# Optimization experiments

Measured on AMD Instinct MI355X. Metric: run time of the kernel, lower is better.

## Reference

```python
import jax, jax.numpy as jnp
import numpy as np

N, D_IN, UNITS = 8192, 2048, 2048


def setup_inputs() -> dict:
    key = jax.random.key(0)
    ks = jax.random.split(key, 14)
    s_in = 1.0 / np.sqrt(D_IN)
    s_u = 1.0 / np.sqrt(UNITS)
    return {
        "x": jax.random.normal(ks[0], (N, UNITS), jnp.float32),
        "y": jax.random.normal(ks[1], (N, D_IN), jnp.float32),
        # W* act on y (D_IN -> UNITS), U* act on x (UNITS -> UNITS)
        "Wz": jax.random.normal(ks[2], (D_IN, UNITS), jnp.float32) * s_in,
        "bz": jnp.zeros((UNITS,), jnp.float32),
        "Uz": jax.random.normal(ks[3], (UNITS, UNITS), jnp.float32) * s_u,
        "buz": jax.random.normal(ks[4], (UNITS,), jnp.float32) * 0.05,  # glorot-init bias
        "Wr": jax.random.normal(ks[5], (D_IN, UNITS), jnp.float32) * s_in,
        "br": jnp.zeros((UNITS,), jnp.float32),
        "Ur": jax.random.normal(ks[6], (UNITS, UNITS), jnp.float32) * s_u,
        "bur": jnp.zeros((UNITS,), jnp.float32),
        "Wg": jax.random.normal(ks[7], (D_IN, UNITS), jnp.float32) * s_in,
        "bg": jax.random.normal(ks[8], (UNITS,), jnp.float32) * 0.05,  # glorot-init bias
        "Ug": jax.random.normal(ks[9], (UNITS, UNITS), jnp.float32) * s_u,
        "bug": jnp.zeros((UNITS,), jnp.float32),
    }


def reference(x, y, Wz, bz, Uz, buz, Wr, br, Ur, bur, Wg, bg, Ug, bug):
    # Batch the three y-projections and the two x-projections into single GEMMs.
    Wy = y @ jnp.concatenate([Wz, Wr, Wg], axis=1)          # [N, 3*UNITS]
    Ux = x @ jnp.concatenate([Uz, Ur], axis=1)               # [N, 2*UNITS]
    u = Wz.shape[1]
    z = Wy[:, :u] + bz + Ux[:, :u] + buz                     # NOTE: no sigmoid (faithful to source)
    r = Wy[:, u:2 * u] + br + Ux[:, u:] + bur                # NOTE: no sigmoid (faithful to source)
    h = jnp.tanh(Wy[:, 2 * u:] + bg + (r * x) @ Ug + bug)
    return (1.0 - z) * x + z * h
```

## Files before the change

### kernel.cpp

```cpp
#include <hip/hip_runtime.h>
#include <hip/hip_bf16.h>
#include <cstdint>
#include <cmath>

typedef __bf16 bf16;
typedef __bf16 bf16x8 __attribute__((ext_vector_type(8)));
typedef __bf16 bf16x4 __attribute__((ext_vector_type(4)));
typedef __bf16 bf16x2 __attribute__((ext_vector_type(2)));
typedef float f32x4 __attribute__((ext_vector_type(4)));

#define NROWS 8192
#define UNITS 2048
#define NT 64
#define NSPLIT 32

__device__ __forceinline__ void gload_lds16(const bf16* g, const bf16* lds) {
  __builtin_amdgcn_global_load_lds(
      (const __attribute__((address_space(1))) uint32_t*)(uintptr_t)g,
      (__attribute__((address_space(3))) uint32_t*)(uint32_t)(uintptr_t)lds,
      16, 0, 0);
}

#define BARR do { asm volatile("" ::: "memory"); __builtin_amdgcn_s_barrier(); \
                  asm volatile("" ::: "memory"); } while (0)
#define SCHEDB do { asm volatile("" ::: "memory"); __builtin_amdgcn_sched_barrier(0); \
                    asm volatile("" ::: "memory"); } while (0)
#define WAITV(N) asm volatile("s_waitcnt vmcnt(" #N ")" ::: "memory")

__device__ __forceinline__ float fast_tanh(float v) {
  float e = __expf(2.f * v);
  return 1.f - 2.f / (e + 1.f);
}

__global__ void pack_xy_kernel(const float* __restrict__ x, const float* __restrict__ y,
                               bf16* __restrict__ xb, bf16* __restrict__ yb) {
  size_t n4 = (size_t)NROWS * UNITS / 4;
  size_t stride = (size_t)gridDim.x * blockDim.x;
  for (size_t i = (size_t)blockIdx.x * blockDim.x + threadIdx.x; i < n4; i += stride) {
    float4 vx = ((const float4*)x)[i];
    float4 vy = ((const float4*)y)[i];
    bf16x4 ox = {(bf16)vx.x, (bf16)vx.y, (bf16)vx.z, (bf16)vx.w};
    bf16x4 oy = {(bf16)vy.x, (bf16)vy.y, (bf16)vy.z, (bf16)vy.w};
    ((bf16x4*)xb)[i] = ox;
    ((bf16x4*)yb)[i] = oy;
  }
}

__global__ void transpose_cvt6_kernel(const float* __restrict__ Wz, const float* __restrict__ Uz,
                                      const float* __restrict__ Wr, const float* __restrict__ Ur,
                                      const float* __restrict__ Wg, const float* __restrict__ Ug,
                                      bf16* __restrict__ Bzr, bf16* __restrict__ Bgt) {
  __shared__ float t[64][33];
  const float* src;
  bf16* dst;
  int koff;
  switch (blockIdx.z) {
    case 0: src = Wz; dst = Bzr;                         koff = 0;    break;
    case 1: src = Uz; dst = Bzr;                         koff = 2048; break;
    case 2: src = Wr; dst = Bzr + (size_t)2048 * 4096;   koff = 0;    break;
    case 3: src = Ur; dst = Bzr + (size_t)2048 * 4096;   koff = 2048; break;
    case 4: src = Wg; dst = Bgt;                         koff = 0;    break;
    default: src = Ug; dst = Bgt;                        koff = 2048; break;
  }
  int j0 = blockIdx.x * 32, k0 = blockIdx.y * 64;
  int tx = threadIdx.x & 31, ty = threadIdx.x >> 5;
#pragma unroll
  for (int i = 0; i < 64; i += 8)
    t[ty + i][tx] = src[(size_t)(k0 + ty + i) * UNITS + j0 + tx];
  __syncthreads();
#pragma unroll
  for (int i = 0; i < 32; i += 8) {
    int j = j0 + ty + i;
    bf16x2 v = {(bf16)t[2 * tx][ty + i], (bf16)t[2 * tx + 1][ty + i]};
    *(bf16x2*)&dst[(size_t)j * 4096 + koff + k0 + 2 * tx] = v;
  }
}

template <int EPI>
__global__ __launch_bounds__(512, 2)
void gemm256(const bf16* __restrict__ A0, const bf16* __restrict__ A1,
             const bf16* __restrict__ Bt,
             const float* __restrict__ bias_a, const float* __restrict__ bias_b,
             const float* __restrict__ bias_c, const float* __restrict__ bias_d,
             const bf16* __restrict__ xin, bf16* __restrict__ zbuf,
             bf16* __restrict__ rxbuf, float* __restrict__ outbuf) {
  __shared__ bf16 LDS[2][32768];
  const int tid = threadIdx.x;
  const int wv = tid >> 6, lane = tid & 63;
  const int wr = wv >> 2, wc = wv & 3;

  const int nl = (int)gridDim.x >> 3;
  const int xc = (int)blockIdx.x & 7;
  const int l = (int)blockIdx.x >> 3;
  const int bxq = nl >> 4;
  const int by = (xc & 1) * 16 + (l & 15);
  const int bx = (xc >> 1) * bxq + (l >> 4);
  const int brow = by * 256;
  const int bcol = bx * 256;

  const int rr = lane >> 2;
  const int kk_st = ((lane & 3) * 8) ^ ((rr & 6) << 2);
  int offA[2][2], offB[2][2], dstA[2][2], dstB[2][2];
#pragma unroll
  for (int H = 0; H < 2; ++H)
#pragma unroll
    for (int c = 0; c < 2; ++c) {
      int ssA = H * 8 + wv;
      offA[H][c] = (brow + c * 128 + (ssA >> 1) * 16 + rr) * 2048 + (ssA & 1) * 32 + kk_st;
      dstA[H][c] = c * 8192 + ssA * 512;
      int ssB = (wv >> 2) * 8 + H * 4 + (wv & 3);
      offB[H][c] = (bcol + c * 128 + (ssB >> 1) * 16 + rr) * 4096 + (ssB & 1) * 32 + kk_st;
      dstB[H][c] = 16384 + c * 8192 + ssB * 512;
    }

  const int lr = lane & 15;
  const int kread = ((lane >> 4) * 8) ^ ((lr & 6) << 2);
  const int abase = wr * 8192 + lr * 32 + kread;
  const int bbase = 16384 + (wc >> 1) * 8192 + (wc & 1) * 4096 + lr * 32 + kread;

#define ST_A(TI, H, BUF)                                                      \
  if ((TI) < NT) {                                                            \
    const bf16* _s = ((TI) < NSPLIT) ? A0 + (size_t)(TI)*64                   \
                                     : A1 + (size_t)((TI)-NSPLIT) * 64;       \
    gload_lds16(_s + offA[H][0], (BUF) + dstA[H][0]);                         \
    gload_lds16(_s + offA[H][1], (BUF) + dstA[H][1]);                         \
  }
#define ST_B(TI, H, BUF)                                                      \
  if ((TI) < NT) {                                                            \
    const bf16* _s = Bt + (size_t)(TI)*64;                                    \
    gload_lds16(_s + offB[H][0], (BUF) + dstB[H][0]);                         \
    gload_lds16(_s + offB[H][1], (BUF) + dstB[H][1]);                         \
  }
#define RD_B(DST, LP, NB)                                                     \
  _Pragma("unroll") for (int kh = 0; kh < 2; ++kh)                            \
  _Pragma("unroll") for (int n = 0; n < 2; ++n)                               \
      DST[n][kh] = *(const bf16x8*)((LP) + bbase + ((n + 2 * (NB)) * 2 + kh) * 512);
#define RD_A(DST, LP, MB)                                                     \
  _Pragma("unroll") for (int kh = 0; kh < 2; ++kh)                            \
  _Pragma("unroll") for (int m = 0; m < 4; ++m)                               \
      DST[m][kh] = *(const bf16x8*)((LP) + abase + ((m + 4 * (MB)) * 2 + kh) * 512);
#define MFMA_Q(AARR, BARR_, MOFF, NOFF)                                       \
  __builtin_amdgcn_s_setprio(1);                                              \
  _Pragma("unroll") for (int kh = 0; kh < 2; ++kh)                            \
  _Pragma("unroll") for (int m = 0; m < 4; ++m)                               \
  _Pragma("unroll") for (int n = 0; n < 2; ++n)                               \
      acc[m + MOFF][n + NOFF] = __builtin_amdgcn_mfma_f32_16x16x32_bf16(      \
          AARR[m][kh], BARR_[n][kh], acc[m + MOFF][n + NOFF], 0, 0, 0);       \
  __builtin_amdgcn_s_setprio(0);

  f32x4 acc[8][4];
#pragma unroll
  for (int m = 0; m < 8; ++m)
#pragma unroll
    for (int n = 0; n < 4; ++n) {
      f32x4 zz = {0.f, 0.f, 0.f, 0.f};
      acc[m][n] = zz;
    }

  bf16x8 a0[4][2], a1[4][2], b0[2][2], b1[2][2];

  {
    bf16* L0 = &LDS[0][0];
    bf16* L1 = &LDS[1][0];
    ST_A(0, 0, L0); ST_B(0, 0, L0); ST_A(0, 1, L0); ST_B(0, 1, L0);
    ST_B(1, 0, L1); ST_A(1, 0, L1);
    WAITV(4);
    BARR;
  }

#define TILE(T, CUR, NXT, WB)                                                 \
  {                                                                           \
    const bf16* Lc = &LDS[CUR][0];                                            \
    bf16* Lcw = &LDS[CUR][0];                                                 \
    bf16* Lnw = &LDS[NXT][0];                                                 \
                                                                     \
    ST_A((T) + 1, 1, Lnw);                                                    \
    ST_B((T) + 1, 1, Lnw);                                                    \
    RD_A(a0, Lc, 0);                                                          \
    RD_B(b0, Lc, 0);                                                          \
    RD_B(b1, Lc, 1);                                                          \
    SCHEDB;                                                                   \
    MFMA_Q(a0, b0, 0, 0);                                                     \
    MFMA_Q(a0, b1, 0, 2);                                                     \
    BARR;                                                                     \
                                                                     \
    ST_B((T) + 2, 0, Lcw);                                                    \
    ST_A((T) + 2, 0, Lcw);                                                    \
    RD_A(a1, Lc, 1);                                                          \
    SCHEDB;                                                                   \
    MFMA_Q(a1, b0, 4, 0);                                                     \
    MFMA_Q(a1, b1, 4, 2);                                                     \
    WAITV(WB); BARR;                                                          \
  }

#pragma unroll 1
  for (int t = 0; t < NT - 2; t += 2) {
    TILE(t, 0, 1, 4);
    TILE(t + 1, 1, 0, 4);
  }
  TILE(NT - 2, 0, 1, 0);
  TILE(NT - 1, 1, 0, 0);

  const int lq = (lane >> 4) << 2;
  const int lc = lane & 15;
  const int rowb = brow + wr * 128;
  const int colb = bcol + wc * 64;
  if constexpr (EPI == 0) {
    if (bcol < UNITS) {
#pragma unroll
      for (int m = 0; m < 8; ++m)
#pragma unroll
        for (int n = 0; n < 4; ++n) {
          int col = colb + n * 16 + lc;
          float ba = bias_a[col] + bias_b[col];
#pragma unroll
          for (int q = 0; q < 4; ++q) {
            int row = rowb + m * 16 + lq + q;
            zbuf[(size_t)row * UNITS + col] = (bf16)(acc[m][n][q] + ba);
          }
        }
    } else {
#pragma unroll
      for (int m = 0; m < 8; ++m)
#pragma unroll
        for (int n = 0; n < 4; ++n) {
          int col = colb - UNITS + n * 16 + lc;
          float bc = bias_c[col] + bias_d[col];
#pragma unroll
          for (int q = 0; q < 4; ++q) {
            int row = rowb + m * 16 + lq + q;
            size_t idx = (size_t)row * UNITS + col;
            float r = acc[m][n][q] + bc;
            rxbuf[idx] = (bf16)(r * (float)xin[idx]);
          }
        }
    }
  } else {
#pragma unroll
    for (int m = 0; m < 8; ++m)
#pragma unroll
      for (int n = 0; n < 4; ++n) {
        int col = colb + n * 16 + lc;
        float bg_ = bias_a[col] + bias_b[col];
#pragma unroll
        for (int q = 0; q < 4; ++q) {
          int row = rowb + m * 16 + lq + q;
          size_t idx = (size_t)row * UNITS + col;
          float h = fast_tanh(acc[m][n][q] + bg_);
          float zv = (float)zbuf[idx];
          float xv = (float)xin[idx];
          outbuf[idx] = (1.f - zv) * xv + zv * h;
        }
      }
  }
#undef ST_A
#undef ST_B
#undef RD_A
#undef RD_B
#undef MFMA_Q
#undef TILE
}

extern "C" void kernel_launch(void* const* d_in, const int* in_sizes, int n_in,
                              void* d_out, int out_size, void* d_ws, size_t ws_size,
                              hipStream_t stream) {
  const float* x   = (const float*)d_in[0];
  const float* y   = (const float*)d_in[1];
  const float* Wz  = (const float*)d_in[2];
  const float* bz  = (const float*)d_in[3];
  const float* Uz  = (const float*)d_in[4];
  const float* buz = (const float*)d_in[5];
  const float* Wr  = (const float*)d_in[6];
  const float* br  = (const float*)d_in[7];
  const float* Ur  = (const float*)d_in[8];
  const float* bur = (const float*)d_in[9];
  const float* Wg  = (const float*)d_in[10];
  const float* bg  = (const float*)d_in[11];
  const float* Ug  = (const float*)d_in[12];
  const float* bug = (const float*)d_in[13];
  float* out = (float*)d_out;

  char* w = (char*)d_ws;
  bf16* Ybf = (bf16*)w;  w += (size_t)NROWS * UNITS * 2;
  bf16* Xbf = (bf16*)w;  w += (size_t)NROWS * UNITS * 2;
  bf16* RX  = (bf16*)w;  w += (size_t)NROWS * UNITS * 2;
  bf16* Bzr = (bf16*)w;  w += (size_t)4096 * 4096 * 2;
  bf16* Bgt = (bf16*)w;  w += (size_t)2048 * 4096 * 2;
  bf16* Zb  = (bf16*)w;  w += (size_t)NROWS * UNITS * 2;

  pack_xy_kernel<<<2048, 256, 0, stream>>>(x, y, Xbf, Ybf);
  dim3 tg(64, 32, 6);
  transpose_cvt6_kernel<<<tg, 256, 0, stream>>>(Wz, Uz, Wr, Ur, Wg, Ug, Bzr, Bgt);

  gemm256<0><<<512, 512, 0, stream>>>(Ybf, Xbf, Bzr, bz, buz, br, bur, Xbf, Zb, RX, nullptr);
  gemm256<1><<<256, 512, 0, stream>>>(Ybf, RX, Bgt, bg, bug, nullptr, nullptr, Xbf, Zb, nullptr, out);
}
```

Baseline: 421.5 us.

## Use 16 waves per 256x256 GEMM tile, halving per-wave work

Doubles the workgroup to 1024 threads (16 waves in a 4x4 arrangement), so each wave owns a 64x64 sub-tile instead of 128x64. The global-to-LDS staging is reassigned so each wave issues one 16-byte load per half instead of two, and the wait counts are adjusted to match. The aim is more latency hiding per CU and lower accumulator register pressure. In exchange the LDS reuse ratio per wave drops, there are more barrier participants, and occupancy drops to one block per CU at 128KB LDS.

```diff
diff --git a/kernel.cpp b/kernel.cpp
--- a/kernel.cpp
+++ b/kernel.cpp
@@ -77,7 +77,7 @@
 }
 
 template <int EPI>
-__global__ __launch_bounds__(512, 2)
+__global__ __launch_bounds__(1024)
 void gemm256(const bf16* __restrict__ A0, const bf16* __restrict__ A1,
              const bf16* __restrict__ Bt,
              const float* __restrict__ bias_a, const float* __restrict__ bias_b,
@@ -86,8 +86,9 @@
              bf16* __restrict__ rxbuf, float* __restrict__ outbuf) {
   __shared__ bf16 LDS[2][32768];
   const int tid = threadIdx.x;
-  const int wv = tid >> 6, lane = tid & 63;
-  const int wr = wv >> 2, wc = wv & 3;
+  const int lane = tid & 63;
+  const int wvu = __builtin_amdgcn_readfirstlane(tid >> 6);
+  const int wr = wvu >> 2, wc = wvu & 3;
 
   const int nl = (int)gridDim.x >> 3;
   const int xc = (int)blockIdx.x & 7;
@@ -100,36 +101,33 @@
 
   const int rr = lane >> 2;
   const int kk_st = ((lane & 3) * 8) ^ ((rr & 6) << 2);
-  int offA[2][2], offB[2][2], dstA[2][2], dstB[2][2];
-#pragma unroll
-  for (int H = 0; H < 2; ++H)
-#pragma unroll
-    for (int c = 0; c < 2; ++c) {
-      int ssA = H * 8 + wv;
-      offA[H][c] = (brow + c * 128 + (ssA >> 1) * 16 + rr) * 2048 + (ssA & 1) * 32 + kk_st;
-      dstA[H][c] = c * 8192 + ssA * 512;
-      int ssB = (wv >> 2) * 8 + H * 4 + (wv & 3);
-      offB[H][c] = (bcol + c * 128 + (ssB >> 1) * 16 + rr) * 4096 + (ssB & 1) * 32 + kk_st;
-      dstB[H][c] = 16384 + c * 8192 + ssB * 512;
-    }
+  const int laneA = rr * 2048 + kk_st;
+  const int laneB = rr * 4096 + kk_st;
+  int uniA[2], uniB[2], dstA[2], dstB[2];
+#pragma unroll
+  for (int H = 0; H < 2; ++H) {
+    int ss = (wvu >> 2) * 8 + H * 4 + (wvu & 3);
+    uniA[H] = (brow + (ss >> 1) * 16) * 2048 + (ss & 1) * 32;
+    dstA[H] = ss * 512;
+    uniB[H] = (bcol + (ss >> 1) * 16) * 4096 + (ss & 1) * 32;
+    dstB[H] = 16384 + ss * 512;
+  }
 
   const int lr = lane & 15;
   const int kread = ((lane >> 4) * 8) ^ ((lr & 6) << 2);
-  const int abase = wr * 8192 + lr * 32 + kread;
-  const int bbase = 16384 + (wc >> 1) * 8192 + (wc & 1) * 4096 + lr * 32 + kread;
+  const int abase = wr * 4096 + lr * 32 + kread;
+  const int bbase = 16384 + wc * 4096 + lr * 32 + kread;
 
 #define ST_A(TI, H, BUF)                                                      \
   if ((TI) < NT) {                                                            \
     const bf16* _s = ((TI) < NSPLIT) ? A0 + (size_t)(TI)*64                   \
                                      : A1 + (size_t)((TI)-NSPLIT) * 64;       \
-    gload_lds16(_s + offA[H][0], (BUF) + dstA[H][0]);                         \
-    gload_lds16(_s + offA[H][1], (BUF) + dstA[H][1]);                         \
+    gload_lds16(_s + uniA[H] + laneA, (BUF) + dstA[H]);                       \
   }
 #define ST_B(TI, H, BUF)                                                      \
   if ((TI) < NT) {                                                            \
     const bf16* _s = Bt + (size_t)(TI)*64;                                    \
-    gload_lds16(_s + offB[H][0], (BUF) + dstB[H][0]);                         \
-    gload_lds16(_s + offB[H][1], (BUF) + dstB[H][1]);                         \
+    gload_lds16(_s + uniB[H] + laneB, (BUF) + dstB[H]);                       \
   }
 #define RD_B(DST, LP, NB)                                                     \
   _Pragma("unroll") for (int kh = 0; kh < 2; ++kh)                            \
@@ -137,34 +135,34 @@
       DST[n][kh] = *(const bf16x8*)((LP) + bbase + ((n + 2 * (NB)) * 2 + kh) * 512);
 #define RD_A(DST, LP, MB)                                                     \
   _Pragma("unroll") for (int kh = 0; kh < 2; ++kh)                            \
-  _Pragma("unroll") for (int m = 0; m < 4; ++m)                               \
-      DST[m][kh] = *(const bf16x8*)((LP) + abase + ((m + 4 * (MB)) * 2 + kh) * 512);
+  _Pragma("unroll") for (int m = 0; m < 2; ++m)                               \
+      DST[m][kh] = *(const bf16x8*)((LP) + abase + ((m + 2 * (MB)) * 2 + kh) * 512);
 #define MFMA_Q(AARR, BARR_, MOFF, NOFF)                                       \
   __builtin_amdgcn_s_setprio(1);                                              \
   _Pragma("unroll") for (int kh = 0; kh < 2; ++kh)                            \
-  _Pragma("unroll") for (int m = 0; m < 4; ++m)                               \
+  _Pragma("unroll") for (int m = 0; m < 2; ++m)                               \
   _Pragma("unroll") for (int n = 0; n < 2; ++n)                               \
       acc[m + MOFF][n + NOFF] = __builtin_amdgcn_mfma_f32_16x16x32_bf16(      \
           AARR[m][kh], BARR_[n][kh], acc[m + MOFF][n + NOFF], 0, 0, 0);       \
   __builtin_amdgcn_s_setprio(0);
 
-  f32x4 acc[8][4];
-#pragma unroll
-  for (int m = 0; m < 8; ++m)
+  f32x4 acc[4][4];
+#pragma unroll
+  for (int m = 0; m < 4; ++m)
 #pragma unroll
     for (int n = 0; n < 4; ++n) {
       f32x4 zz = {0.f, 0.f, 0.f, 0.f};
       acc[m][n] = zz;
     }
 
-  bf16x8 a0[4][2], a1[4][2], b0[2][2], b1[2][2];
+  bf16x8 a0[2][2], a1[2][2], b0[2][2], b1[2][2];
 
   {
     bf16* L0 = &LDS[0][0];
     bf16* L1 = &LDS[1][0];
     ST_A(0, 0, L0); ST_B(0, 0, L0); ST_A(0, 1, L0); ST_B(0, 1, L0);
     ST_B(1, 0, L1); ST_A(1, 0, L1);
-    WAITV(4);
+    WAITV(2);
     BARR;
   }
 
@@ -188,27 +186,27 @@
     ST_A((T) + 2, 0, Lcw);                                                    \
     RD_A(a1, Lc, 1);                                                          \
     SCHEDB;                                                                   \
-    MFMA_Q(a1, b0, 4, 0);                                                     \
-    MFMA_Q(a1, b1, 4, 2);                                                     \
+    MFMA_Q(a1, b0, 2, 0);                                                     \
+    MFMA_Q(a1, b1, 2, 2);                                                     \
     WAITV(WB); BARR;                                                          \
   }
 
 #pragma unroll 1
   for (int t = 0; t < NT - 2; t += 2) {
-    TILE(t, 0, 1, 4);
-    TILE(t + 1, 1, 0, 4);
+    TILE(t, 0, 1, 2);
+    TILE(t + 1, 1, 0, 2);
   }
   TILE(NT - 2, 0, 1, 0);
   TILE(NT - 1, 1, 0, 0);
 
   const int lq = (lane >> 4) << 2;
   const int lc = lane & 15;
-  const int rowb = brow + wr * 128;
+  const int rowb = brow + wr * 64;
   const int colb = bcol + wc * 64;
   if constexpr (EPI == 0) {
     if (bcol < UNITS) {
 #pragma unroll
-      for (int m = 0; m < 8; ++m)
+      for (int m = 0; m < 4; ++m)
 #pragma unroll
         for (int n = 0; n < 4; ++n) {
           int col = colb + n * 16 + lc;
@@ -221,7 +219,7 @@
         }
     } else {
 #pragma unroll
-      for (int m = 0; m < 8; ++m)
+      for (int m = 0; m < 4; ++m)
 #pragma unroll
         for (int n = 0; n < 4; ++n) {
           int col = colb - UNITS + n * 16 + lc;
@@ -237,7 +235,7 @@
     }
   } else {
 #pragma unroll
-    for (int m = 0; m < 8; ++m)
+    for (int m = 0; m < 4; ++m)
 #pragma unroll
       for (int n = 0; n < 4; ++n) {
         int col = colb + n * 16 + lc;
@@ -292,6 +290,6 @@
   dim3 tg(64, 32, 6);
   transpose_cvt6_kernel<<<tg, 256, 0, stream>>>(Wz, Uz, Wr, Ur, Wg, Ug, Bzr, Bgt);
 
-  gemm256<0><<<512, 512, 0, stream>>>(Ybf, Xbf, Bzr, bz, buz, br, bur, Xbf, Zb, RX, nullptr);
-  gemm256<1><<<256, 512, 0, stream>>>(Ybf, RX, Bgt, bg, bug, nullptr, nullptr, Xbf, Zb, nullptr, out);
-}
+  gemm256<0><<<512, 1024, 0, stream>>>(Ybf, Xbf, Bzr, bz, buz, br, bur, Xbf, Zb, RX, nullptr);
+  gemm256<1><<<256, 1024, 0, stream>>>(Ybf, RX, Bgt, bg, bug, nullptr, nullptr, Xbf, Zb, nullptr, out);
+}
```

Result: no change. 425.9 us (+1.0%).

## Use 16-wave 1024-thread blocks for the first fused GEMM

Applied to the files above, without the earlier changes.

Adds a gemm16w variant that computes each 256x256 tile with 16 waves of 64x64 instead of 8 waves of 128x64. Each wave now issues one global->LDS load per half-stage instead of two, and holds half the accumulator and A-fragment registers. The first GEMM launches with 1024 threads per block while the second keeps the original 8-wave kernel. This cuts per-wave register pressure and adds more waves to hide latency, at the cost of more LDS B-fragment reads per MFMA and only one block per CU given the 128KB LDS footprint.

```diff
diff --git a/kernel.cpp b/kernel.cpp
--- a/kernel.cpp
+++ b/kernel.cpp
@@ -77,8 +77,8 @@
 }
 
 template <int EPI>
-__global__ __launch_bounds__(512, 2)
-void gemm256(const bf16* __restrict__ A0, const bf16* __restrict__ A1,
+__global__ __launch_bounds__(1024)
+void gemm16w(const bf16* __restrict__ A0, const bf16* __restrict__ A1,
              const bf16* __restrict__ Bt,
              const float* __restrict__ bias_a, const float* __restrict__ bias_b,
              const float* __restrict__ bias_c, const float* __restrict__ bias_d,
@@ -86,8 +86,9 @@
              bf16* __restrict__ rxbuf, float* __restrict__ outbuf) {
   __shared__ bf16 LDS[2][32768];
   const int tid = threadIdx.x;
-  const int wv = tid >> 6, lane = tid & 63;
-  const int wr = wv >> 2, wc = wv & 3;
+  const int lane = tid & 63;
+  const int wvu = __builtin_amdgcn_readfirstlane(tid >> 6);
+  const int wr = wvu >> 2, wc = wvu & 3;
 
   const int nl = (int)gridDim.x >> 3;
   const int xc = (int)blockIdx.x & 7;
@@ -100,36 +101,33 @@
 
   const int rr = lane >> 2;
   const int kk_st = ((lane & 3) * 8) ^ ((rr & 6) << 2);
-  int offA[2][2], offB[2][2], dstA[2][2], dstB[2][2];
-#pragma unroll
-  for (int H = 0; H < 2; ++H)
-#pragma unroll
-    for (int c = 0; c < 2; ++c) {
-      int ssA = H * 8 + wv;
-      offA[H][c] = (brow + c * 128 + (ssA >> 1) * 16 + rr) * 2048 + (ssA & 1) * 32 + kk_st;
-      dstA[H][c] = c * 8192 + ssA * 512;
-      int ssB = (wv >> 2) * 8 + H * 4 + (wv & 3);
-      offB[H][c] = (bcol + c * 128 + (ssB >> 1) * 16 + rr) * 4096 + (ssB & 1) * 32 + kk_st;
-      dstB[H][c] = 16384 + c * 8192 + ssB * 512;
-    }
+  const int laneA = rr * 2048 + kk_st;
+  const int laneB = rr * 4096 + kk_st;
+  int uniA[2], uniB[2], dstA[2], dstB[2];
+#pragma unroll
+  for (int H = 0; H < 2; ++H) {
+    int ss = (wvu >> 2) * 8 + H * 4 + (wvu & 3);
+    uniA[H] = (brow + (ss >> 1) * 16) * 2048 + (ss & 1) * 32;
+    dstA[H] = ss * 512;
+    uniB[H] = (bcol + (ss >> 1) * 16) * 4096 + (ss & 1) * 32;
+    dstB[H] = 16384 + ss * 512;
+  }
 
   const int lr = lane & 15;
   const int kread = ((lane >> 4) * 8) ^ ((lr & 6) << 2);
-  const int abase = wr * 8192 + lr * 32 + kread;
-  const int bbase = 16384 + (wc >> 1) * 8192 + (wc & 1) * 4096 + lr * 32 + kread;
+  const int abase = wr * 4096 + lr * 32 + kread;
+  const int bbase = 16384 + wc * 4096 + lr * 32 + kread;
 
 #define ST_A(TI, H, BUF)                                                      \
   if ((TI) < NT) {                                                            \
     const bf16* _s = ((TI) < NSPLIT) ? A0 + (size_t)(TI)*64                   \
                                      : A1 + (size_t)((TI)-NSPLIT) * 64;       \
-    gload_lds16(_s + offA[H][0], (BUF) + dstA[H][0]);                         \
-    gload_lds16(_s + offA[H][1], (BUF) + dstA[H][1]);                         \
+    gload_lds16(_s + uniA[H] + laneA, (BUF) + dstA[H]);                       \
   }
 #define ST_B(TI, H, BUF)                                                      \
   if ((TI) < NT) {                                                            \
     const bf16* _s = Bt + (size_t)(TI)*64;                                    \
-    gload_lds16(_s + offB[H][0], (BUF) + dstB[H][0]);                         \
-    gload_lds16(_s + offB[H][1], (BUF) + dstB[H][1]);                         \
+    gload_lds16(_s + uniB[H] + laneB, (BUF) + dstB[H]);                       \
   }
 #define RD_B(DST, LP, NB)                                                     \
   _Pragma("unroll") for (int kh = 0; kh < 2; ++kh)                            \
@@ -137,34 +135,34 @@
       DST[n][kh] = *(const bf16x8*)((LP) + bbase + ((n + 2 * (NB)) * 2 + kh) * 512);
 #define RD_A(DST, LP, MB)                                                     \
   _Pragma("unroll") for (int kh = 0; kh < 2; ++kh)                            \
-  _Pragma("unroll") for (int m = 0; m < 4; ++m)                               \
-      DST[m][kh] = *(const bf16x8*)((LP) + abase + ((m + 4 * (MB)) * 2 + kh) * 512);
+  _Pragma("unroll") for (int m = 0; m < 2; ++m)                               \
+      DST[m][kh] = *(const bf16x8*)((LP) + abase + ((m + 2 * (MB)) * 2 + kh) * 512);
 #define MFMA_Q(AARR, BARR_, MOFF, NOFF)                                       \
   __builtin_amdgcn_s_setprio(1);                                              \
   _Pragma("unroll") for (int kh = 0; kh < 2; ++kh)                            \
-  _Pragma("unroll") for (int m = 0; m < 4; ++m)                               \
+  _Pragma("unroll") for (int m = 0; m < 2; ++m)                               \
   _Pragma("unroll") for (int n = 0; n < 2; ++n)                               \
       acc[m + MOFF][n + NOFF] = __builtin_amdgcn_mfma_f32_16x16x32_bf16(      \
           AARR[m][kh], BARR_[n][kh], acc[m + MOFF][n + NOFF], 0, 0, 0);       \
   __builtin_amdgcn_s_setprio(0);
 
-  f32x4 acc[8][4];
-#pragma unroll
-  for (int m = 0; m < 8; ++m)
+  f32x4 acc[4][4];
+#pragma unroll
+  for (int m = 0; m < 4; ++m)
 #pragma unroll
     for (int n = 0; n < 4; ++n) {
       f32x4 zz = {0.f, 0.f, 0.f, 0.f};
       acc[m][n] = zz;
     }
 
-  bf16x8 a0[4][2], a1[4][2], b0[2][2], b1[2][2];
+  bf16x8 a0[2][2], a1[2][2], b0[2][2], b1[2][2];
 
   {
     bf16* L0 = &LDS[0][0];
     bf16* L1 = &LDS[1][0];
     ST_A(0, 0, L0); ST_B(0, 0, L0); ST_A(0, 1, L0); ST_B(0, 1, L0);
     ST_B(1, 0, L1); ST_A(1, 0, L1);
-    WAITV(4);
+    WAITV(2);
     BARR;
   }
 
@@ -173,7 +171,6 @@
     const bf16* Lc = &LDS[CUR][0];                                            \
     bf16* Lcw = &LDS[CUR][0];                                                 \
     bf16* Lnw = &LDS[NXT][0];                                                 \
-                                                                     \
     ST_A((T) + 1, 1, Lnw);                                                    \
     ST_B((T) + 1, 1, Lnw);                                                    \
     RD_A(a0, Lc, 0);                                                          \
@@ -183,7 +180,189 @@
     MFMA_Q(a0, b0, 0, 0);                                                     \
     MFMA_Q(a0, b1, 0, 2);                                                     \
     BARR;                                                                     \
-                                                                     \
+    ST_B((T) + 2, 0, Lcw);                                                    \
+    ST_A((T) + 2, 0, Lcw);                                                    \
+    RD_A(a1, Lc, 1);                                                          \
+    SCHEDB;                                                                   \
+    MFMA_Q(a1, b0, 2, 0);                                                     \
+    MFMA_Q(a1, b1, 2, 2);                                                     \
+    WAITV(WB); BARR;                                                          \
+  }
+
+#pragma unroll 1
+  for (int t = 0; t < NT - 2; t += 2) {
+    TILE(t, 0, 1, 2);
+    TILE(t + 1, 1, 0, 2);
+  }
+  TILE(NT - 2, 0, 1, 0);
+  TILE(NT - 1, 1, 0, 0);
+
+  const int lq = (lane >> 4) << 2;
+  const int lc = lane & 15;
+  const int rowb = brow + wr * 64;
+  const int colb = bcol + wc * 64;
+  if constexpr (EPI == 0) {
+    if (bcol < UNITS) {
+#pragma unroll
+      for (int m = 0; m < 4; ++m)
+#pragma unroll
+        for (int n = 0; n < 4; ++n) {
+          int col = colb + n * 16 + lc;
+          float ba = bias_a[col] + bias_b[col];
+#pragma unroll
+          for (int q = 0; q < 4; ++q) {
+            int row = rowb + m * 16 + lq + q;
+            zbuf[(size_t)row * UNITS + col] = (bf16)(acc[m][n][q] + ba);
+          }
+        }
+    } else {
+#pragma unroll
+      for (int m = 0; m < 4; ++m)
+#pragma unroll
+        for (int n = 0; n < 4; ++n) {
+          int col = colb - UNITS + n * 16 + lc;
+          float bc = bias_c[col] + bias_d[col];
+#pragma unroll
+          for (int q = 0; q < 4; ++q) {
+            int row = rowb + m * 16 + lq + q;
+            size_t idx = (size_t)row * UNITS + col;
+            float r = acc[m][n][q] + bc;
+            rxbuf[idx] = (bf16)(r * (float)xin[idx]);
+          }
+        }
+    }
+  } else {
+#pragma unroll
+    for (int m = 0; m < 4; ++m)
+#pragma unroll
+      for (int n = 0; n < 4; ++n) {
+        int col = colb + n * 16 + lc;
+        float bg_ = bias_a[col] + bias_b[col];
+#pragma unroll
+        for (int q = 0; q < 4; ++q) {
+          int row = rowb + m * 16 + lq + q;
+          size_t idx = (size_t)row * UNITS + col;
+          float h = fast_tanh(acc[m][n][q] + bg_);
+          float zv = (float)zbuf[idx];
+          float xv = (float)xin[idx];
+          outbuf[idx] = (1.f - zv) * xv + zv * h;
+        }
+      }
+  }
+#undef ST_A
+#undef ST_B
+#undef RD_A
+#undef RD_B
+#undef MFMA_Q
+#undef TILE
+}
+
+template <int EPI>
+__global__ __launch_bounds__(512, 2)
+void gemm8w(const bf16* __restrict__ A0, const bf16* __restrict__ A1,
+            const bf16* __restrict__ Bt,
+            const float* __restrict__ bias_a, const float* __restrict__ bias_b,
+            const float* __restrict__ bias_c, const float* __restrict__ bias_d,
+            const bf16* __restrict__ xin, bf16* __restrict__ zbuf,
+            bf16* __restrict__ rxbuf, float* __restrict__ outbuf) {
+  __shared__ bf16 LDS[2][32768];
+  const int tid = threadIdx.x;
+  const int wv = tid >> 6, lane = tid & 63;
+  const int wr = wv >> 2, wc = wv & 3;
+
+  const int nl = (int)gridDim.x >> 3;
+  const int xc = (int)blockIdx.x & 7;
+  const int l = (int)blockIdx.x >> 3;
+  const int bxq = nl >> 4;
+  const int by = (xc & 1) * 16 + (l & 15);
+  const int bx = (xc >> 1) * bxq + (l >> 4);
+  const int brow = by * 256;
+  const int bcol = bx * 256;
+
+  const int rr = lane >> 2;
+  const int kk_st = ((lane & 3) * 8) ^ ((rr & 6) << 2);
+  int offA[2][2], offB[2][2], dstA[2][2], dstB[2][2];
+#pragma unroll
+  for (int H = 0; H < 2; ++H)
+#pragma unroll
+    for (int c = 0; c < 2; ++c) {
+      int ssA = H * 8 + wv;
+      offA[H][c] = (brow + c * 128 + (ssA >> 1) * 16 + rr) * 2048 + (ssA & 1) * 32 + kk_st;
+      dstA[H][c] = c * 8192 + ssA * 512;
+      int ssB = (wv >> 2) * 8 + H * 4 + (wv & 3);
+      offB[H][c] = (bcol + c * 128 + (ssB >> 1) * 16 + rr) * 4096 + (ssB & 1) * 32 + kk_st;
+      dstB[H][c] = 16384 + c * 8192 + ssB * 512;
+    }
+
+  const int lr = lane & 15;
+  const int kread = ((lane >> 4) * 8) ^ ((lr & 6) << 2);
+  const int abase = wr * 8192 + lr * 32 + kread;
+  const int bbase = 16384 + (wc >> 1) * 8192 + (wc & 1) * 4096 + lr * 32 + kread;
+
+#define ST_A(TI, H, BUF)                                                      \
+  if ((TI) < NT) {                                                            \
+    const bf16* _s = ((TI) < NSPLIT) ? A0 + (size_t)(TI)*64                   \
+                                     : A1 + (size_t)((TI)-NSPLIT) * 64;       \
+    gload_lds16(_s + offA[H][0], (BUF) + dstA[H][0]);                         \
+    gload_lds16(_s + offA[H][1], (BUF) + dstA[H][1]);                         \
+  }
+#define ST_B(TI, H, BUF)                                                      \
+  if ((TI) < NT) {                                                            \
+    const bf16* _s = Bt + (size_t)(TI)*64;                                    \
+    gload_lds16(_s + offB[H][0], (BUF) + dstB[H][0]);                         \
+    gload_lds16(_s + offB[H][1], (BUF) + dstB[H][1]);                         \
+  }
+#define RD_B(DST, LP, NB)                                                     \
+  _Pragma("unroll") for (int kh = 0; kh < 2; ++kh)                            \
+  _Pragma("unroll") for (int n = 0; n < 2; ++n)                               \
+      DST[n][kh] = *(const bf16x8*)((LP) + bbase + ((n + 2 * (NB)) * 2 + kh) * 512);
+#define RD_A(DST, LP, MB)                                                     \
+  _Pragma("unroll") for (int kh = 0; kh < 2; ++kh)                            \
+  _Pragma("unroll") for (int m = 0; m < 4; ++m)                               \
+      DST[m][kh] = *(const bf16x8*)((LP) + abase + ((m + 4 * (MB)) * 2 + kh) * 512);
+#define MFMA_Q(AARR, BARR_, MOFF, NOFF)                                       \
+  __builtin_amdgcn_s_setprio(1);                                              \
+  _Pragma("unroll") for (int kh = 0; kh < 2; ++kh)                            \
+  _Pragma("unroll") for (int m = 0; m < 4; ++m)                               \
+  _Pragma("unroll") for (int n = 0; n < 2; ++n)                               \
+      acc[m + MOFF][n + NOFF] = __builtin_amdgcn_mfma_f32_16x16x32_bf16(      \
+          AARR[m][kh], BARR_[n][kh], acc[m + MOFF][n + NOFF], 0, 0, 0);       \
+  __builtin_amdgcn_s_setprio(0);
+
+  f32x4 acc[8][4];
+#pragma unroll
+  for (int m = 0; m < 8; ++m)
+#pragma unroll
+    for (int n = 0; n < 4; ++n) {
+      f32x4 zz = {0.f, 0.f, 0.f, 0.f};
+      acc[m][n] = zz;
+    }
+
+  bf16x8 a0[4][2], a1[4][2], b0[2][2], b1[2][2];
+
+  {
+    bf16* L0 = &LDS[0][0];
+    bf16* L1 = &LDS[1][0];
+    ST_A(0, 0, L0); ST_B(0, 0, L0); ST_A(0, 1, L0); ST_B(0, 1, L0);
+    ST_B(1, 0, L1); ST_A(1, 0, L1);
+    WAITV(4);
+    BARR;
+  }
+
+#define TILE(T, CUR, NXT, WB)                                                 \
+  {                                                                           \
+    const bf16* Lc = &LDS[CUR][0];                                            \
+    bf16* Lcw = &LDS[CUR][0];                                                 \
+    bf16* Lnw = &LDS[NXT][0];                                                 \
+    ST_A((T) + 1, 1, Lnw);                                                    \
+    ST_B((T) + 1, 1, Lnw);                                                    \
+    RD_A(a0, Lc, 0);                                                          \
+    RD_B(b0, Lc, 0);                                                          \
+    RD_B(b1, Lc, 1);                                                          \
+    SCHEDB;                                                                   \
+    MFMA_Q(a0, b0, 0, 0);                                                     \
+    MFMA_Q(a0, b1, 0, 2);                                                     \
+    BARR;                                                                     \
     ST_B((T) + 2, 0, Lcw);                                                    \
     ST_A((T) + 2, 0, Lcw);                                                    \
     RD_A(a1, Lc, 1);                                                          \
@@ -292,6 +471,6 @@
   dim3 tg(64, 32, 6);
   transpose_cvt6_kernel<<<tg, 256, 0, stream>>>(Wz, Uz, Wr, Ur, Wg, Ug, Bzr, Bgt);
 
-  gemm256<0><<<512, 512, 0, stream>>>(Ybf, Xbf, Bzr, bz, buz, br, bur, Xbf, Zb, RX, nullptr);
-  gemm256<1><<<256, 512, 0, stream>>>(Ybf, RX, Bgt, bg, bug, nullptr, nullptr, Xbf, Zb, nullptr, out);
-}
+  gemm16w<0><<<512, 1024, 0, stream>>>(Ybf, Xbf, Bzr, bz, buz, br, bur, Xbf, Zb, RX, nullptr);
+  gemm8w<1><<<256, 512, 0, stream>>>(Ybf, RX, Bgt, bg, bug, nullptr, nullptr, Xbf, Zb, nullptr, out);
+}
```

Measured after the change: 435.5 us. 1.03x slower.
